# Kernel tuning notes

Hardware: AMD Instinct MI355X
Metric: run time of the kernel (lower is better)

## Reference

```python
import jax, jax.numpy as jnp
import numpy as np


def setup_inputs() -> dict:
    key = jax.random.key(0)
    k1, k2 = jax.random.split(key)
    x = jax.random.normal(k1, (4, 2048, 512), dtype=jnp.float32)
    proxy = jax.random.normal(k2, (16, 512), dtype=jnp.float32)
    return {"x": x, "proxy": proxy}


def reference(x, proxy):
    # x: (B, S, D), proxy: (P, D)
    num_proxies = proxy.shape[0]
    # prods: (B, P, S) = proxy @ x^T per batch
    prods = jnp.einsum('pd,bsd->bps', proxy, x)
    # broadcast outer product: (B, P, S, D), then running prefix sum over seq
    y = jnp.cumsum(prods[..., None] * x[:, None, :, :], axis=2)
    # softmax gate over proxies (dim=1), scaled by sqrt(P)
    w = jax.nn.softmax(prods / jnp.sqrt(jnp.float32(num_proxies)), axis=1)
    # weighted sum over proxies -> (B, S, D)
    out = jnp.einsum('bps,bpsd->bsd', w, y)
    return out
```

## Files before the change

### kernel.cpp

```cpp
#include <hip/hip_runtime.h>
#include <hip/hip_bf16.h>

#define B 4
#define S 2048
#define D 512
#define P 16
#define NC 64
#define CL 32

__global__ __launch_bounds__(256) void k_prods(const float* __restrict__ x,
                                               const float* __restrict__ proxy,
                                               float* __restrict__ prods,
                                               float* __restrict__ wgt) {
    int wid  = (blockIdx.x * blockDim.x + threadIdx.x) >> 6;
    int lane = threadIdx.x & 63;
    if (wid >= B * S) return;

    const float* xr = x + (size_t)wid * D + lane * 8;
    float4 xa = *(const float4*)xr;
    float4 xb = *(const float4*)(xr + 4);

    float part[P];
#pragma unroll
    for (int p = 0; p < P; ++p) {
        const float* pr = proxy + p * D + lane * 8;
        float4 pa = *(const float4*)pr;
        float4 pb = *(const float4*)(pr + 4);
        part[p] = xa.x*pa.x + xa.y*pa.y + xa.z*pa.z + xa.w*pa.w
                + xb.x*pb.x + xb.y*pb.y + xb.z*pb.z + xb.w*pb.w;
    }
#pragma unroll
    for (int p = 0; p < P; ++p) {
        float v = part[p];
#pragma unroll
        for (int off = 32; off > 0; off >>= 1) v += __shfl_xor(v, off);
        part[p] = v;
    }
    float m = part[0];
#pragma unroll
    for (int p = 1; p < P; ++p) m = fmaxf(m, part[p]);
    float e[P];
    float den = 0.f;
#pragma unroll
    for (int p = 0; p < P; ++p) { e[p] = __expf((part[p] - m) * 0.25f); den += e[p]; }
    float inv = 1.f / den;

    int lp = lane & 15;
    float myp = part[0], mye = e[0];
#pragma unroll
    for (int p = 1; p < P; ++p) {
        bool sel = (lp == p);
        myp = sel ? part[p] : myp;
        mye = sel ? e[p]    : mye;
    }
    if (lane < P) {
        prods[(size_t)wid * P + lane] = myp;
        wgt  [(size_t)wid * P + lane] = mye * inv;
    }
}

__global__ __launch_bounds__(512) void k_totals(const float* __restrict__ x,
                                                const float* __restrict__ prods,
                                                float* __restrict__ T) {
    int c = blockIdx.x & (NC - 1);
    int b = blockIdx.x >> 6;
    int d = threadIdx.x;

    float acc[P];
#pragma unroll
    for (int p = 0; p < P; ++p) acc[p] = 0.f;

    int bs0 = b * S + c * CL;
#pragma unroll 4
    for (int i = 0; i < CL; ++i) {
        int bs = bs0 + i;
        float xv = x[(size_t)bs * D + d];
        const float4* pp = (const float4*)(prods + (size_t)bs * P);
        float pr[P];
        ((float4*)pr)[0] = pp[0];
        ((float4*)pr)[1] = pp[1];
        ((float4*)pr)[2] = pp[2];
        ((float4*)pr)[3] = pp[3];
#pragma unroll
        for (int p = 0; p < P; ++p) acc[p] = fmaf(pr[p], xv, acc[p]);
    }
    size_t tb = ((size_t)(b * NC + c)) * (P * D) + d;
#pragma unroll
    for (int p = 0; p < P; ++p) T[tb + p * D] = acc[p];
}

__global__ __launch_bounds__(256) void k_scan(float* __restrict__ T) {
    int t = blockIdx.x * blockDim.x + threadIdx.x;
    int d = t & (D - 1);
    int p = (t >> 9) & (P - 1);
    int b = t >> 13;
    size_t base = ((size_t)b * NC * P + p) * D + d;
    float run = 0.f;
#pragma unroll 8
    for (int c = 0; c < NC; ++c) {
        size_t idx = base + (size_t)c * (P * D);
        float v = T[idx];
        T[idx] = run;
        run += v;
    }
}

__global__ __launch_bounds__(512) void k_apply(const float* __restrict__ x,
                                               const float* __restrict__ prods,
                                               const float* __restrict__ wgt,
                                               const float* __restrict__ T,
                                               float* __restrict__ out) {
    int c = blockIdx.x & (NC - 1);
    int b = blockIdx.x >> 6;
    int d = threadIdx.x;

    float st[P];
    size_t tb = ((size_t)(b * NC + c)) * (P * D) + d;
#pragma unroll
    for (int p = 0; p < P; ++p) st[p] = T[tb + p * D];

    int bs0 = b * S + c * CL;
#pragma unroll 2
    for (int i = 0; i < CL; ++i) {
        int bs = bs0 + i;
        float xv = x[(size_t)bs * D + d];
        const float4* pp = (const float4*)(prods + (size_t)bs * P);
        const float4* wp = (const float4*)(wgt   + (size_t)bs * P);
        float pr[P], ww[P];
        ((float4*)pr)[0] = pp[0];
        ((float4*)pr)[1] = pp[1];
        ((float4*)pr)[2] = pp[2];
        ((float4*)pr)[3] = pp[3];
        ((float4*)ww)[0] = wp[0];
        ((float4*)ww)[1] = wp[1];
        ((float4*)ww)[2] = wp[2];
        ((float4*)ww)[3] = wp[3];
        float o = 0.f;
#pragma unroll
        for (int p = 0; p < P; ++p) {
            st[p] = fmaf(pr[p], xv, st[p]);
            o = fmaf(ww[p], st[p], o);
        }
        out[(size_t)bs * D + d] = o;
    }
}

extern "C" void kernel_launch(void* const* d_in, const int* in_sizes, int n_in,
                              void* d_out, int out_size, void* d_ws, size_t ws_size,
                              hipStream_t stream) {
    const float* x     = (const float*)d_in[0];
    const float* proxy = (const float*)d_in[1];
    float* out   = (float*)d_out;

    float* prods = (float*)d_ws;
    float* wgt   = prods + (size_t)B * S * P;
    float* T     = wgt   + (size_t)B * S * P;

    k_prods <<<(B * S) / 4, 256, 0, stream>>>(x, proxy, prods, wgt);
    k_totals<<<B * NC,     512, 0, stream>>>(x, prods, T);
    k_scan  <<<(B * P * D) / 256, 256, 0, stream>>>(T);
    k_apply <<<B * NC,     512, 0, stream>>>(x, prods, wgt, T, out);
}
```

Before: 40.92 us.

## Fuse prods, totals, scan, apply into one cooperative kernel with grid syncs

Merges the four kernels into a single cooperatively launched kernel. Per-chunk projections and softmax weights are computed into shared memory and reused in the totals and apply phases, and grid-wide syncs separate the chunk scan. This removes three kernel launches and the global round trip for prods and weights. In exchange it adds two grid barriers, and the projection phase and scan run with fewer active blocks.

```diff
diff --git a/kernel.cpp b/kernel.cpp
--- a/kernel.cpp
+++ b/kernel.cpp
@@ -1,5 +1,8 @@
 #include <hip/hip_runtime.h>
 #include <hip/hip_bf16.h>
+#include <hip/hip_cooperative_groups.h>
+
+namespace cg = cooperative_groups;
 
 #define B 4
 #define S 2048
@@ -8,140 +11,123 @@
 #define NC 64
 #define CL 32
 
-__global__ __launch_bounds__(256) void k_prods(const float* __restrict__ x,
-                                               const float* __restrict__ proxy,
-                                               float* __restrict__ prods,
-                                               float* __restrict__ wgt) {
-    int wid  = (blockIdx.x * blockDim.x + threadIdx.x) >> 6;
-    int lane = threadIdx.x & 63;
-    if (wid >= B * S) return;
+__global__ __launch_bounds__(512) void fused(const float* __restrict__ x,
+                                             const float* __restrict__ proxy,
+                                             float* __restrict__ T,
+                                             float* __restrict__ out) {
+    __shared__ float s_pr[CL][P];
+    __shared__ float s_w [CL][P];
 
-    const float* xr = x + (size_t)wid * D + lane * 8;
-    float4 xa = *(const float4*)xr;
-    float4 xb = *(const float4*)(xr + 4);
+    const int c    = blockIdx.x & (NC - 1);
+    const int b    = blockIdx.x >> 6;
+    const int tid  = threadIdx.x;
+    const int lane = tid & 63;
+    const int wv   = tid >> 6;
+    const int bs0  = b * S + c * CL;
 
-    float part[P];
 #pragma unroll
-    for (int p = 0; p < P; ++p) {
-        const float* pr = proxy + p * D + lane * 8;
-        float4 pa = *(const float4*)pr;
-        float4 pb = *(const float4*)(pr + 4);
-        part[p] = xa.x*pa.x + xa.y*pa.y + xa.z*pa.z + xa.w*pa.w
-                + xb.x*pb.x + xb.y*pb.y + xb.z*pb.z + xb.w*pb.w;
-    }
-#pragma unroll
-    for (int p = 0; p < P; ++p) {
-        float v = part[p];
-#pragma unroll
-        for (int off = 32; off > 0; off >>= 1) v += __shfl_xor(v, off);
-        part[p] = v;
-    }
-    float m = part[0];
-#pragma unroll
-    for (int p = 1; p < P; ++p) m = fmaxf(m, part[p]);
-    float e[P];
-    float den = 0.f;
-#pragma unroll
-    for (int p = 0; p < P; ++p) { e[p] = __expf((part[p] - m) * 0.25f); den += e[p]; }
-    float inv = 1.f / den;
+    for (int r = 0; r < 4; ++r) {
+        const int sl = wv * 4 + r;
+        const int bs = bs0 + sl;
+        const float* xr = x + (size_t)bs * D + lane * 8;
+        float4 xa = *(const float4*)xr;
+        float4 xb = *(const float4*)(xr + 4);
 
-    int lp = lane & 15;
-    float myp = part[0], mye = e[0];
-#pragma unroll
-    for (int p = 1; p < P; ++p) {
-        bool sel = (lp == p);
-        myp = sel ? part[p] : myp;
-        mye = sel ? e[p]    : mye;
-    }
-    if (lane < P) {
-        prods[(size_t)wid * P + lane] = myp;
-        wgt  [(size_t)wid * P + lane] = mye * inv;
-    }
-}
-
-__global__ __launch_bounds__(512) void k_totals(const float* __restrict__ x,
-                                                const float* __restrict__ prods,
-                                                float* __restrict__ T) {
-    int c = blockIdx.x & (NC - 1);
-    int b = blockIdx.x >> 6;
-    int d = threadIdx.x;
-
-    float acc[P];
-#pragma unroll
-    for (int p = 0; p < P; ++p) acc[p] = 0.f;
-
-    int bs0 = b * S + c * CL;
-#pragma unroll 4
-    for (int i = 0; i < CL; ++i) {
-        int bs = bs0 + i;
-        float xv = x[(size_t)bs * D + d];
-        const float4* pp = (const float4*)(prods + (size_t)bs * P);
-        float pr[P];
-        ((float4*)pr)[0] = pp[0];
-        ((float4*)pr)[1] = pp[1];
-        ((float4*)pr)[2] = pp[2];
-        ((float4*)pr)[3] = pp[3];
-#pragma unroll
-        for (int p = 0; p < P; ++p) acc[p] = fmaf(pr[p], xv, acc[p]);
-    }
-    size_t tb = ((size_t)(b * NC + c)) * (P * D) + d;
-#pragma unroll
-    for (int p = 0; p < P; ++p) T[tb + p * D] = acc[p];
-}
-
-__global__ __launch_bounds__(256) void k_scan(float* __restrict__ T) {
-    int t = blockIdx.x * blockDim.x + threadIdx.x;
-    int d = t & (D - 1);
-    int p = (t >> 9) & (P - 1);
-    int b = t >> 13;
-    size_t base = ((size_t)b * NC * P + p) * D + d;
-    float run = 0.f;
-#pragma unroll 8
-    for (int c = 0; c < NC; ++c) {
-        size_t idx = base + (size_t)c * (P * D);
-        float v = T[idx];
-        T[idx] = run;
-        run += v;
-    }
-}
-
-__global__ __launch_bounds__(512) void k_apply(const float* __restrict__ x,
-                                               const float* __restrict__ prods,
-                                               const float* __restrict__ wgt,
-                                               const float* __restrict__ T,
-                                               float* __restrict__ out) {
-    int c = blockIdx.x & (NC - 1);
-    int b = blockIdx.x >> 6;
-    int d = threadIdx.x;
-
-    float st[P];
-    size_t tb = ((size_t)(b * NC + c)) * (P * D) + d;
-#pragma unroll
-    for (int p = 0; p < P; ++p) st[p] = T[tb + p * D];
-
-    int bs0 = b * S + c * CL;
-#pragma unroll 2
-    for (int i = 0; i < CL; ++i) {
-        int bs = bs0 + i;
-        float xv = x[(size_t)bs * D + d];
-        const float4* pp = (const float4*)(prods + (size_t)bs * P);
-        const float4* wp = (const float4*)(wgt   + (size_t)bs * P);
-        float pr[P], ww[P];
-        ((float4*)pr)[0] = pp[0];
-        ((float4*)pr)[1] = pp[1];
-        ((float4*)pr)[2] = pp[2];
-        ((float4*)pr)[3] = pp[3];
-        ((float4*)ww)[0] = wp[0];
-        ((float4*)ww)[1] = wp[1];
-        ((float4*)ww)[2] = wp[2];
-        ((float4*)ww)[3] = wp[3];
-        float o = 0.f;
+        float part[P];
 #pragma unroll
         for (int p = 0; p < P; ++p) {
-            st[p] = fmaf(pr[p], xv, st[p]);
-            o = fmaf(ww[p], st[p], o);
+            const float* pr = proxy + p * D + lane * 8;
+            float4 pa = *(const float4*)pr;
+            float4 pb = *(const float4*)(pr + 4);
+            part[p] = xa.x*pa.x + xa.y*pa.y + xa.z*pa.z + xa.w*pa.w
+                    + xb.x*pb.x + xb.y*pb.y + xb.z*pb.z + xb.w*pb.w;
         }
-        out[(size_t)bs * D + d] = o;
+#pragma unroll
+        for (int p = 0; p < P; ++p) {
+            float v = part[p];
+#pragma unroll
+            for (int off = 32; off > 0; off >>= 1) v += __shfl_xor(v, off);
+            part[p] = v;
+        }
+        float m = part[0];
+#pragma unroll
+        for (int p = 1; p < P; ++p) m = fmaxf(m, part[p]);
+        float e[P];
+        float den = 0.f;
+#pragma unroll
+        for (int p = 0; p < P; ++p) { e[p] = __expf((part[p] - m) * 0.25f); den += e[p]; }
+        float inv = 1.f / den;
+
+        int lp = lane & 15;
+        float myp = part[0], mye = e[0];
+#pragma unroll
+        for (int p = 1; p < P; ++p) {
+            bool sel = (lp == p);
+            myp = sel ? part[p] : myp;
+            mye = sel ? e[p]    : mye;
+        }
+        if (lane < P) {
+            s_pr[sl][lane] = myp;
+            s_w [sl][lane] = mye * inv;
+        }
+    }
+    __syncthreads();
+
+    {
+        const int d = tid;
+        float acc[P];
+#pragma unroll
+        for (int p = 0; p < P; ++p) acc[p] = 0.f;
+#pragma unroll 4
+        for (int i = 0; i < CL; ++i) {
+            float xv = x[(size_t)(bs0 + i) * D + d];
+#pragma unroll
+            for (int p = 0; p < P; ++p) acc[p] = fmaf(s_pr[i][p], xv, acc[p]);
+        }
+        size_t tb = (size_t)blockIdx.x * (P * D) + d;
+#pragma unroll
+        for (int p = 0; p < P; ++p) T[tb + p * D] = acc[p];
+    }
+
+    cg::this_grid().sync();
+
+    if (blockIdx.x < (B * P * D) / 512) {
+        int t  = blockIdx.x * 512 + tid;
+        int d  = t & (D - 1);
+        int p  = (t >> 9) & (P - 1);
+        int bb = t >> 13;
+        size_t base = ((size_t)bb * NC * P + p) * D + d;
+        float run = 0.f;
+#pragma unroll 8
+        for (int cc = 0; cc < NC; ++cc) {
+            size_t idx = base + (size_t)cc * (P * D);
+            float v = T[idx];
+            T[idx] = run;
+            run += v;
+        }
+    }
+
+    cg::this_grid().sync();
+
+    {
+        const int d = tid;
+        float st[P];
+        size_t tb = (size_t)blockIdx.x * (P * D) + d;
+#pragma unroll
+        for (int p = 0; p < P; ++p) st[p] = T[tb + p * D];
+
+#pragma unroll 2
+        for (int i = 0; i < CL; ++i) {
+            const int bs = bs0 + i;
+            float xv = x[(size_t)bs * D + d];
+            float o = 0.f;
+#pragma unroll
+            for (int p = 0; p < P; ++p) {
+                st[p] = fmaf(s_pr[i][p], xv, st[p]);
+                o = fmaf(s_w[i][p], st[p], o);
+            }
+            out[(size_t)bs * D + d] = o;
+        }
     }
 }
 
@@ -150,14 +136,9 @@
                               hipStream_t stream) {
     const float* x     = (const float*)d_in[0];
     const float* proxy = (const float*)d_in[1];
-    float* out   = (float*)d_out;
+    float* out = (float*)d_out;
+    float* T   = (float*)d_ws;
 
-    float* prods = (float*)d_ws;
-    float* wgt   = prods + (size_t)B * S * P;
-    float* T     = wgt   + (size_t)B * S * P;
-
-    k_prods <<<(B * S) / 4, 256, 0, stream>>>(x, proxy, prods, wgt);
-    k_totals<<<B * NC,     512, 0, stream>>>(x, prods, T);
-    k_scan  <<<(B * P * D) / 256, 256, 0, stream>>>(T);
-    k_apply <<<B * NC,     512, 0, stream>>>(x, prods, wgt, T, out);
+    void* args[] = { (void*)&x, (void*)&proxy, (void*)&T, (void*)&out };
+    hipLaunchCooperativeKernel((void*)fused, dim3(B * NC), dim3(512), args, 0, stream);
 }
```

Result: slower. 112.4 us (+174.7%).
